# Performance work log

Measured on AMD Instinct MI355X. Metric: run time of the kernel, lower is better.

The kernel has to match this reference:

```python
import jax, jax.numpy as jnp
import numpy as np

B, I, O, E = 1024, 512, 512, 16


def setup_inputs() -> dict:
    key = jax.random.key(0)
    k_x, k_c, k_w = jax.random.split(key, 3)
    x = jax.random.normal(k_x, (B, I), dtype=jnp.float32)
    coeffs = jax.random.uniform(k_c, (B, E), dtype=jnp.float32)
    expert_weights = jax.random.normal(k_w, (E, I, O), dtype=jnp.float32) * 0.01
    expert_biases = jnp.zeros((E, O), dtype=jnp.float32)
    return {"x": x, "coeffs": coeffs, "expert_weights": expert_weights, "expert_biases": expert_biases}


def reference(x, coeffs, expert_weights, expert_biases):
    # Soft-MoE: per-sample convex blend of expert linear layers.
    # Equivalent to out[b] = x[b] @ (sum_e coeffs[b,e] * W[e]) + sum_e coeffs[b,e] * b[e]
    # Contract x with each expert first (avoids the [B,I,O] combined-weight tensor).
    per_expert = jnp.einsum('bi,eio->beo', x, expert_weights)   # [B,E,O]
    out = jnp.einsum('be,beo->bo', coeffs, per_expert)          # [B,O]
    out = out + coeffs @ expert_biases                          # [B,O]
    return out
```

## Files before the change

### kernel.cpp

```cpp
#include <hip/hip_runtime.h>

#define B_  1024
#define I_  512
#define O_  512
#define E_  16
#define K_  8192

#define BK 64
#define NSTEP (I_ / BK)
#define NWG  (E_ * (B_ / 128) * (O_ / 128))

typedef __attribute__((ext_vector_type(8))) short short8;
typedef __attribute__((ext_vector_type(8))) unsigned short ushort8;
typedef __attribute__((ext_vector_type(4))) unsigned short ushort4v;
typedef __attribute__((ext_vector_type(4))) float f32x4;

__device__ __forceinline__ unsigned short f2bf(float f) {
  union { float f; unsigned u; } v; v.f = f;
  unsigned r = v.u + 0x7fffu + ((v.u >> 16) & 1u);
  return (unsigned short)(r >> 16);
}
__device__ __forceinline__ float bf2f(unsigned short h) {
  union { unsigned u; float f; } v; v.u = ((unsigned)h) << 16;
  return v.f;
}

__device__ __forceinline__ void gload_lds16(const unsigned short* g, unsigned short* l) {
  __builtin_amdgcn_global_load_lds(
      (const __attribute__((address_space(1))) void*)g,
      (__attribute__((address_space(3))) void*)l, 16, 0, 0);
}

__global__ void prep_kernel(const float* __restrict__ x,
                            const float* __restrict__ W,
                            unsigned short* __restrict__ xb,
                            unsigned short* __restrict__ Wt) {
  __shared__ unsigned short tile[64][65];
  if (blockIdx.x < 256) {
    int base = (blockIdx.x * 256 + threadIdx.x) * 8;
    const float4* xp = (const float4*)(x + base);
    float4 v0 = xp[0], v1 = xp[1];
    ushort8 r;
    r[0] = f2bf(v0.x); r[1] = f2bf(v0.y); r[2] = f2bf(v0.z); r[3] = f2bf(v0.w);
    r[4] = f2bf(v1.x); r[5] = f2bf(v1.y); r[6] = f2bf(v1.z); r[7] = f2bf(v1.w);
    *(ushort8*)(xb + base) = r;
  } else {
    int bw = blockIdx.x - 256;
    int kt = (bw & 127) << 6;
    int nt = (bw >> 7) << 6;
    int t = threadIdx.x;
#pragma unroll
    for (int it = 0; it < 16; ++it) {
      int idx = it * 256 + t;
      int r = idx >> 6, c = idx & 63;
      tile[r][c] = f2bf(W[(long)(kt + r) * O_ + nt + c]);
    }
    __syncthreads();
#pragma unroll
    for (int it = 0; it < 2; ++it) {
      int idx = it * 256 + t;
      int r2 = idx >> 3;
      int c2 = (idx & 7) * 8;
      ushort8 v;
#pragma unroll
      for (int j = 0; j < 8; ++j) v[j] = tile[c2 + j][r2];
      *(ushort8*)(Wt + (long)(nt + r2) * K_ + kt + c2) = v;
    }
  }
}

__global__ void bias_init_kernel(const float* __restrict__ coeffs,
                                 const float* __restrict__ eb,
                                 float* __restrict__ out) {
  int t = blockIdx.x * 256 + threadIdx.x;
  int b = t >> 7;
  int o4 = (t & 127) * 4;
  const float* cb = coeffs + b * E_;
  float4 acc = {0.f, 0.f, 0.f, 0.f};
#pragma unroll
  for (int e = 0; e < E_; ++e) {
    float c = cb[e];
    float4 bv = *(const float4*)(eb + e * O_ + o4);
    acc.x += c * bv.x; acc.y += c * bv.y; acc.z += c * bv.z; acc.w += c * bv.w;
  }
  *(float4*)(out + b * O_ + o4) = acc;
}

template <int USE_PART>
__global__ __launch_bounds__(256) void gemm_kernel(
    const unsigned short* __restrict__ xb,
    const unsigned short* __restrict__ Wt,
    const float* __restrict__ coeffs,
    float* __restrict__ out,
    unsigned short* __restrict__ part) {
  __shared__ unsigned short As[2][128 * 64];
  __shared__ unsigned short Bs[2][128 * 64];
  int bx = blockIdx.x;
  int swz = (bx & 7) * (NWG / 8) + (bx >> 3);
  int e = swz >> 5;
  int tile = swz & 31;
  int tm = tile >> 2, tn = tile & 3;
  int brow = tm * 128, bcol = tn * 128;

  int tid = threadIdx.x;
  int lane = tid & 63, wave = tid >> 6;
  int wr = wave >> 1, wc = wave & 1;

  f32x4 acc[4][4];
#pragma unroll
  for (int m = 0; m < 4; ++m)
#pragma unroll
    for (int n = 0; n < 4; ++n) acc[m][n] = (f32x4){0.f, 0.f, 0.f, 0.f};

  int lr8 = lane >> 3;
  int jj = lane & 7;
  int ksrc = (jj ^ lr8) * 8;
  const unsigned short* gA = xb + (long)(brow + lr8) * I_ + ksrc;
  const unsigned short* gB = Wt + (long)(bcol + lr8) * K_ + e * I_ + ksrc;

  auto STAGE = [&](int buf, int s) {
    long kof = (long)s * BK;
#pragma unroll
    for (int i = 0; i < 4; ++i) {
      int chunk = i * 4 + wave;
      gload_lds16(gA + (long)chunk * 8 * I_ + kof, &As[buf][chunk * 512]);
      gload_lds16(gB + (long)chunk * 8 * K_ + kof, &Bs[buf][chunk * 512]);
    }
  };

  auto COMPUTE = [&](int buf) {
#pragma unroll
    for (int kk = 0; kk < 2; ++kk) {
      int kbyte = kk * 64 + (lane >> 4) * 16;
      short8 af[4], bfr[4];
#pragma unroll
      for (int m = 0; m < 4; ++m) {
        int r = wr * 64 + m * 16 + (lane & 15);
        int off = r * 64 + ((kbyte ^ ((r & 7) << 4)) >> 1);
        af[m] = *(const short8*)(&As[buf][off]);
      }
#pragma unroll
      for (int n = 0; n < 4; ++n) {
        int r = wc * 64 + n * 16 + (lane & 15);
        int off = r * 64 + ((kbyte ^ ((r & 7) << 4)) >> 1);
        bfr[n] = *(const short8*)(&Bs[buf][off]);
      }
#pragma unroll
      for (int m = 0; m < 4; ++m)
#pragma unroll
        for (int n = 0; n < 4; ++n)
          acc[m][n] = __builtin_amdgcn_mfma_f32_16x16x32_bf16(af[m], bfr[n], acc[m][n], 0, 0, 0);
    }
  };

  STAGE(0, 0);
  __syncthreads();
#pragma unroll
  for (int s = 0; s < NSTEP; ++s) {
    if (s + 1 < NSTEP) STAGE((s + 1) & 1, s + 1);
    COMPUTE(s & 1);
    __syncthreads();
  }

  int crow = wr * 64 + (lane >> 4) * 4;
  int ccol = wc * 64 + (lane & 15);
  if (USE_PART) {
    unsigned short* pb = part + (long)e * B_ * O_;
#pragma unroll
    for (int m = 0; m < 4; ++m)
#pragma unroll
      for (int n = 0; n < 4; ++n) {
        long rbase = (long)(brow + crow + m * 16) * O_ + bcol + ccol + n * 16;
#pragma unroll
        for (int j = 0; j < 4; ++j)
          pb[rbase + (long)j * O_] = f2bf(acc[m][n][j]);
      }
  } else {
#pragma unroll
    for (int m = 0; m < 4; ++m)
#pragma unroll
      for (int n = 0; n < 4; ++n) {
#pragma unroll
        for (int j = 0; j < 4; ++j) {
          int row = brow + crow + m * 16 + j;
          float c = coeffs[row * E_ + e];
          atomicAdd(out + (long)row * O_ + bcol + ccol + n * 16, c * acc[m][n][j]);
        }
      }
  }
}

__global__ void combine_kernel(const unsigned short* __restrict__ part,
                               const float* __restrict__ coeffs,
                               const float* __restrict__ eb,
                               float* __restrict__ out) {
  int t = blockIdx.x * 256 + threadIdx.x;
  int b = t >> 7;
  int o4 = (t & 127) * 4;
  const float* cb = coeffs + b * E_;
  float4 acc = {0.f, 0.f, 0.f, 0.f};
#pragma unroll
  for (int e = 0; e < E_; ++e) {
    float c = cb[e];
    ushort4v v = *(const ushort4v*)(part + (long)e * B_ * O_ + (long)b * O_ + o4);
    acc.x += c * bf2f(v[0]); acc.y += c * bf2f(v[1]);
    acc.z += c * bf2f(v[2]); acc.w += c * bf2f(v[3]);
    float4 bv = *(const float4*)(eb + e * O_ + o4);
    acc.x += c * bv.x; acc.y += c * bv.y; acc.z += c * bv.z; acc.w += c * bv.w;
  }
  *(float4*)(out + (long)b * O_ + o4) = acc;
}

extern "C" void kernel_launch(void* const* d_in, const int* in_sizes, int n_in,
                              void* d_out, int out_size, void* d_ws, size_t ws_size,
                              hipStream_t stream) {
  const float* x      = (const float*)d_in[0];
  const float* coeffs = (const float*)d_in[1];
  const float* W      = (const float*)d_in[2];
  const float* eb     = (const float*)d_in[3];
  float* out = (float*)d_out;

  size_t xb_bytes   = (size_t)B_ * I_ * 2;
  size_t Wt_bytes   = (size_t)O_ * K_ * 2;
  size_t part_bytes = (size_t)E_ * B_ * O_ * 2;
  unsigned short* xb   = (unsigned short*)d_ws;
  unsigned short* Wt   = (unsigned short*)((char*)d_ws + xb_bytes);
  unsigned short* part = (unsigned short*)((char*)d_ws + xb_bytes + Wt_bytes);
  bool use_part = ws_size >= xb_bytes + Wt_bytes + part_bytes;

  prep_kernel<<<dim3(256 + 1024), 256, 0, stream>>>(x, W, xb, Wt);
  if (use_part) {
    gemm_kernel<1><<<dim3(NWG), 256, 0, stream>>>(xb, Wt, coeffs, out, part);
    combine_kernel<<<dim3(B_ * O_ / 4 / 256), 256, 0, stream>>>(part, coeffs, eb, out);
  } else {
    bias_init_kernel<<<dim3(B_ * O_ / 4 / 256), 256, 0, stream>>>(coeffs, eb, out);
    gemm_kernel<0><<<dim3(NWG), 256, 0, stream>>>(xb, Wt, coeffs, out, part);
  }
}
```

Before: 30.18 us.

## Vectorize prep and combine loads, and use explicit vmcnt waits in GEMM pipeline

```diff
diff --git a/kernel.cpp b/kernel.cpp
--- a/kernel.cpp
+++ b/kernel.cpp
@@ -35,7 +35,7 @@
                             const float* __restrict__ W,
                             unsigned short* __restrict__ xb,
                             unsigned short* __restrict__ Wt) {
-  __shared__ unsigned short tile[64][65];
+  __shared__ unsigned short tile[64][68];
   if (blockIdx.x < 256) {
     int base = (blockIdx.x * 256 + threadIdx.x) * 8;
     const float4* xp = (const float4*)(x + base);
@@ -50,10 +50,13 @@
     int nt = (bw >> 7) << 6;
     int t = threadIdx.x;
 #pragma unroll
-    for (int it = 0; it < 16; ++it) {
-      int idx = it * 256 + t;
-      int r = idx >> 6, c = idx & 63;
-      tile[r][c] = f2bf(W[(long)(kt + r) * O_ + nt + c]);
+    for (int it = 0; it < 4; ++it) {
+      int r = it * 16 + (t >> 4);
+      int c4 = (t & 15) * 4;
+      float4 v = *(const float4*)(W + (long)(kt + r) * O_ + nt + c4);
+      ushort4v u;
+      u[0] = f2bf(v.x); u[1] = f2bf(v.y); u[2] = f2bf(v.z); u[3] = f2bf(v.w);
+      *(ushort4v*)(&tile[r][c4]) = u;
     }
     __syncthreads();
 #pragma unroll
@@ -154,12 +157,18 @@
   };
 
   STAGE(0, 0);
-  __syncthreads();
 #pragma unroll
   for (int s = 0; s < NSTEP; ++s) {
-    if (s + 1 < NSTEP) STAGE((s + 1) & 1, s + 1);
+    if (s + 1 < NSTEP) {
+      STAGE((s + 1) & 1, s + 1);
+      asm volatile("s_waitcnt vmcnt(8)" ::: "memory");
+    } else {
+      asm volatile("s_waitcnt vmcnt(0)" ::: "memory");
+    }
+    __builtin_amdgcn_sched_barrier(0);
+    __builtin_amdgcn_s_barrier();
     COMPUTE(s & 1);
-    __syncthreads();
+    __builtin_amdgcn_s_barrier();
   }
 
   int crow = wr * 64 + (lane >> 4) * 4;
@@ -195,20 +204,25 @@
                                const float* __restrict__ eb,
                                float* __restrict__ out) {
   int t = blockIdx.x * 256 + threadIdx.x;
-  int b = t >> 7;
-  int o4 = (t & 127) * 4;
+  int b = t >> 6;
+  int o8 = (t & 63) * 8;
   const float* cb = coeffs + b * E_;
-  float4 acc = {0.f, 0.f, 0.f, 0.f};
+  float acc[8] = {0.f, 0.f, 0.f, 0.f, 0.f, 0.f, 0.f, 0.f};
 #pragma unroll
   for (int e = 0; e < E_; ++e) {
     float c = cb[e];
-    ushort4v v = *(const ushort4v*)(part + (long)e * B_ * O_ + (long)b * O_ + o4);
-    acc.x += c * bf2f(v[0]); acc.y += c * bf2f(v[1]);
-    acc.z += c * bf2f(v[2]); acc.w += c * bf2f(v[3]);
-    float4 bv = *(const float4*)(eb + e * O_ + o4);
-    acc.x += c * bv.x; acc.y += c * bv.y; acc.z += c * bv.z; acc.w += c * bv.w;
-  }
-  *(float4*)(out + (long)b * O_ + o4) = acc;
+    ushort8 v = *(const ushort8*)(part + (long)e * B_ * O_ + (long)b * O_ + o8);
+#pragma unroll
+    for (int j = 0; j < 8; ++j) acc[j] += c * bf2f(v[j]);
+    float4 b0 = *(const float4*)(eb + e * O_ + o8);
+    float4 b1 = *(const float4*)(eb + e * O_ + o8 + 4);
+    acc[0] += c * b0.x; acc[1] += c * b0.y; acc[2] += c * b0.z; acc[3] += c * b0.w;
+    acc[4] += c * b1.x; acc[5] += c * b1.y; acc[6] += c * b1.z; acc[7] += c * b1.w;
+  }
+  float4 r0 = {acc[0], acc[1], acc[2], acc[3]};
+  float4 r1 = {acc[4], acc[5], acc[6], acc[7]};
+  *(float4*)(out + (long)b * O_ + o8) = r0;
+  *(float4*)(out + (long)b * O_ + o8 + 4) = r1;
 }
 
 extern "C" void kernel_launch(void* const* d_in, const int* in_sizes, int n_in,
@@ -231,7 +245,7 @@
   prep_kernel<<<dim3(256 + 1024), 256, 0, stream>>>(x, W, xb, Wt);
   if (use_part) {
     gemm_kernel<1><<<dim3(NWG), 256, 0, stream>>>(xb, Wt, coeffs, out, part);
-    combine_kernel<<<dim3(B_ * O_ / 4 / 256), 256, 0, stream>>>(part, coeffs, eb, out);
+    combine_kernel<<<dim3(B_ * O_ / 8 / 256), 256, 0, stream>>>(part, coeffs, eb, out);
   } else {
     bias_init_kernel<<<dim3(B_ * O_ / 4 / 256), 256, 0, stream>>>(coeffs, eb, out);
     gemm_kernel<0><<<dim3(NWG), 256, 0, stream>>>(xb, Wt, coeffs, out, part);
```

Measured after the change: 31.74 us. +5.2%, slower.
